# Performance work log

Measured on AMD Instinct MI355X. Metric: run time of the kernel, lower is better.

The kernel has to match this reference:

```python
import jax, jax.numpy as jnp
import numpy as np

B, A, NC, DIR, LMAX, MAXZ, NORB = 8, 64, 128, 4, 2, 10, 14
NF = NC * DIR * (2 * LMAX + 1)   # 2560
O2 = NORB * NORB                 # 196
AO = A * NORB                    # 896
LOG2 = float(np.log(2.0))

def ssp(v):  # spk shifted softplus
    return jax.nn.softplus(v) - LOG2

def setup_inputs():
    key = jax.random.key(0)
    ks = jax.random.split(key, 12)
    Z = jax.random.randint(ks[0], (B, A), 1, MAXZ)
    idx = np.arange(A)
    nbh_np = np.stack([np.delete(idx, i) for i in range(A)], 0)  # [A, A-1]: all atoms except self
    nbh = jnp.asarray(np.broadcast_to(nbh_np[None], (B, A, A - 1)).copy(), dtype=jnp.int32)
    x = jax.random.normal(ks[1], (B, A, NC), jnp.float32)
    Vijkl = jax.random.normal(ks[2], (B, A, A - 1, NF), jnp.float32) * 0.1
    sc = 1.0 / np.sqrt(NF)
    W_off = jax.random.normal(ks[3], (NF, O2), jnp.float32) * sc
    b_off = jnp.zeros((O2,), jnp.float32)
    W_on = jax.random.normal(ks[4], (NF, O2), jnp.float32) * sc
    b_on = jnp.zeros((O2,), jnp.float32)
    W_ovoff = jax.random.normal(ks[5], (NF, O2), jnp.float32) * sc
    b_ovoff = jnp.zeros((O2,), jnp.float32)
    ov_emb = jax.random.normal(ks[6], (MAXZ, O2), jnp.float32) * 0.1  # trainable overlap onsite embedding
    orb_energies = jax.random.normal(ks[7], (MAXZ, NORB), jnp.float32)  # h0 energies
    s0_energies = jnp.ones((MAXZ, NORB), jnp.float32)                   # s0 init = ones
    W1 = jax.random.normal(ks[8], (NC, NC // 2), jnp.float32) / np.sqrt(NC)
    b1 = jnp.zeros((NC // 2,), jnp.float32)
    W2 = jax.random.normal(ks[9], (NC // 2, 1), jnp.float32) / np.sqrt(NC // 2)
    b2 = jnp.zeros((1,), jnp.float32)
    return {"Z": Z, "nbh": nbh, "x": x, "Vijkl": Vijkl,
            "W_off": W_off, "b_off": b_off, "W_on": W_on, "b_on": b_on,
            "W_ovoff": W_ovoff, "b_ovoff": b_ovoff, "ov_emb": ov_emb,
            "orb_energies": orb_energies, "s0_energies": s0_energies,
            "W1": W1, "b1": b1, "W2": W2, "b2": b2}

def reference(Z, nbh, x, Vijkl, W_off, b_off, W_on, b_on, W_ovoff, b_ovoff,
              ov_emb, orb_energies, s0_energies, W1, b1, W2, b2):
    # permutation that reorders neighbor slots (plus appended zero/self slot) into atom order
    ar = jnp.broadcast_to(jnp.arange(A, dtype=nbh.dtype)[None, :, None], (B, A, 1))
    sort_idx = jnp.argsort(jnp.concatenate([nbh, ar], axis=2), axis=2)  # [B,A,A]
    eyeA = jnp.eye(A, dtype=Vijkl.dtype)
    eyeAO = jnp.eye(AO, dtype=Vijkl.dtype)

    def assemble(off, on):
        # off: [B,A,A-1,O2] pair blocks; on: [B,A,O2] onsite blocks
        offz = jnp.concatenate([off, jnp.zeros((B, A, 1, O2), off.dtype)], axis=2)  # zero self block at slot A-1
        offg = jnp.take_along_axis(offz, sort_idx[..., None], axis=2)               # [B,A,A,O2]
        M = offg + eyeA[None, :, :, None] * on[:, :, None, :]
        M = M.reshape(B, A, A, NORB, NORB).transpose(0, 1, 3, 2, 4).reshape(B, AO, AO)
        return 0.5 * (M + M.transpose(0, 2, 1))

    # Hamiltonian: offsite Dense + onsite Dense mean-aggregated over pairs
    H_off = Vijkl @ W_off + b_off                       # [B,A,A-1,O2]
    H_on = jnp.mean(Vijkl @ W_on + b_on, axis=2)        # [B,A,O2]
    H = assemble(H_off, H_on)
    # h0 single-atom diagonal (orb mask is all-active -> full diagonal)
    H = H + eyeAO[None] * orb_energies[Z].reshape(B, 1, AO)

    # Overlap: offsite Dense + onsite embedding lookup
    S_off = Vijkl @ W_ovoff + b_ovoff
    S_on = ov_emb[Z]                                    # [B,A,O2]
    S = assemble(S_off, S_on)
    S = S + eyeAO[None] * s0_energies[Z].reshape(B, 1, AO)

    # energy head: Dense->ssp->Dense->ScaleShift(0,1), sum over atoms
    Ei = ssp(x @ W1 + b1) @ W2 + b2                     # [B,A,1]
    E = jnp.sum(Ei, axis=1)                             # [B,1]
    return H, S, E
```

## Files before the change

kernel.cpp:

```cpp
#include <hip/hip_runtime.h>

#define B_      8
#define A_      64
#define NPAIR   63
#define NC_     128
#define NF_     2560
#define O2_     196
#define NORB_   14
#define AO_     896
#define NCOLS   588
#define NSTORE  392
#define CSTRIDE 400
#define KSTEPS  80
#define BM      126
#define BN      640
#define BSTEP_BYTES 40960

typedef short bf16x8 __attribute__((ext_vector_type(8)));
typedef float f32x4  __attribute__((ext_vector_type(4)));

__device__ __forceinline__ unsigned f2bf(float f) {
    unsigned u = __builtin_bit_cast(unsigned, f);
    return (u + 0x7fffu + ((u >> 16) & 1u)) >> 16;
}

__global__ __launch_bounds__(512)
void prep_energy(const float* __restrict__ W_off, const float* __restrict__ W_ovoff,
                 const float* __restrict__ W_on, unsigned short* __restrict__ Bws,
                 const float* __restrict__ x, const float* __restrict__ W1,
                 const float* __restrict__ b1, const float* __restrict__ W2,
                 const float* __restrict__ b2, float* __restrict__ E) {
    const int t = threadIdx.x;
    if (blockIdx.x < KSTEPS) {
        __shared__ float wt[32 * BN];
        const int ks = blockIdx.x;
        for (int e = t; e < 32 * BN; e += 512) {
            int kl = e / BN, c = e - kl * BN;
            int kg = ks * 32 + kl;
            float v = 0.f;
            if (c < O2_)          v = W_off  [(size_t)kg * O2_ + c];
            else if (c < 2 * O2_) v = W_ovoff[(size_t)kg * O2_ + (c - O2_)];
            else if (c < 3 * O2_) v = W_on   [(size_t)kg * O2_ + (c - 2 * O2_)];
            wt[kl * BN + c] = v;
        }
        __syncthreads();
        unsigned short* out = Bws + (size_t)ks * (BN * 32);
        for (int e = t; e < BN * 4; e += 512) {
            int n = e >> 2, sg = e & 3;
            uint4 w;
            w.x = f2bf(wt[(sg * 8 + 0) * BN + n]) | (f2bf(wt[(sg * 8 + 1) * BN + n]) << 16);
            w.y = f2bf(wt[(sg * 8 + 2) * BN + n]) | (f2bf(wt[(sg * 8 + 3) * BN + n]) << 16);
            w.z = f2bf(wt[(sg * 8 + 4) * BN + n]) | (f2bf(wt[(sg * 8 + 5) * BN + n]) << 16);
            w.w = f2bf(wt[(sg * 8 + 6) * BN + n]) | (f2bf(wt[(sg * 8 + 7) * BN + n]) << 16);
            *(uint4*)(out + (size_t)n * 32 + sg * 8) = w;
        }
    } else {
        __shared__ float partial[8];
        const int b = blockIdx.x - KSTEPS;
        const int lane = t & 63;
        const int w = t >> 6;
        float esum = 0.f;
        for (int aa = 0; aa < 8; ++aa) {
            const int a = w * 8 + aa;
            const float* xr = x + (size_t)(b * A_ + a) * NC_;
            float hj = b1[lane];
            for (int k = 0; k < NC_; ++k) hj = fmaf(xr[k], W1[k * 64 + lane], hj);
            float sp = fmaxf(hj, 0.f) + log1pf(expf(-fabsf(hj))) - 0.69314718055994531f;
            float v = sp * W2[lane];
            for (int off = 32; off; off >>= 1) v += __shfl_down(v, off);
            if (lane == 0) esum += v + b2[0];
        }
        if (lane == 0) partial[w] = esum;
        __syncthreads();
        if (t == 0) {
            float e = 0.f;
            for (int k = 0; k < 8; ++k) e += partial[k];
            E[b] = e;
        }
    }
}

__global__ __launch_bounds__(1024, 4)
void gemm_off(const float* __restrict__ V, const unsigned short* __restrict__ Bws,
              const float* __restrict__ b_off, const float* __restrict__ b_ovoff,
              const float* __restrict__ b_on, float* __restrict__ HSoff,
              float* __restrict__ Hon) {
    __shared__ alignas(16) float          Af32[4][4096];
    __shared__ alignas(16) unsigned short Ab16[3][4096];
    __shared__ float HonLds[2][O2_];

    const int tid  = threadIdx.x;
    const int mt   = blockIdx.x;
    const int lane = tid & 63;
    const int wv   = tid >> 6;
    const int wm   = wv >> 3, wn = wv & 7;
    const int wvu  = __builtin_amdgcn_readfirstlane(wv);
    const bool sthr = tid < BM * 8;

    const float* asrc = V + (size_t)(mt * BM + (tid >> 3)) * NF_ + (tid & 7) * 4;

    const char* bp = (const char*)Bws + (size_t)(wn * 80 + (lane & 15)) * 64 + (lane >> 4) * 16;
#define BFRAG(t_, nf_) (*(const bf16x8*)(bp + (size_t)(t_) * BSTEP_BYTES + (nf_) * 1024))

    f32x4 acc[4][5];
#pragma unroll
    for (int mf = 0; mf < 4; ++mf)
#pragma unroll
        for (int nf = 0; nf < 5; ++nf)
            acc[mf][nf] = (f32x4){0.f, 0.f, 0.f, 0.f};

    auto stage = [&](int slot, int kk) {
        if (sthr)
            __builtin_amdgcn_global_load_lds(
                (const __attribute__((address_space(1))) void*)(asrc + (size_t)kk * 32),
                (__attribute__((address_space(3))) void*)(&Af32[slot][wvu * 256]), 16, 0, 0);
    };

    const int crr = tid >> 3, cq = tid & 7;
    const int csl = ((cq >> 1) + ((crr + (crr >> 2)) & 3)) & 3;
    const unsigned cdst = (unsigned)(crr * 64 + csl * 16 + (cq & 1) * 8);
    auto conv = [&](int fslot, int bslot) {
        if (sthr) {
            float4 cf = *(const float4*)((const char*)&Af32[fslot][0] + tid * 16);
            unsigned lo, hi;
            asm("v_cvt_pk_bf16_f32 %0, %1, %2" : "=v"(lo) : "v"(cf.x), "v"(cf.y));
            asm("v_cvt_pk_bf16_f32 %0, %1, %2" : "=v"(hi) : "v"(cf.z), "v"(cf.w));
            uint2 cw = {lo, hi};
            *(uint2*)((char*)&Ab16[bslot][0] + cdst) = cw;
        }
    };

    const unsigned klo4 = (unsigned)(lane >> 4);
#define AFRAG(abf_, mf_, Bb16_) {                                                   \
    const unsigned R_ = (unsigned)(wm * 64 + (lane & 15) + (mf_) * 16);             \
    const unsigned sl_ = (klo4 + ((R_ + (R_ >> 2)) & 3)) & 3;                       \
    abf_ = *(const bf16x8*)((const char*)(Bb16_) + R_ * 64 + sl_ * 16); }

#define MFMA1(abf_, bq_, mf_, nf_) \
    acc[mf_][nf_] = __builtin_amdgcn_mfma_f32_16x16x32_bf16(abf_, bq_, acc[mf_][nf_], 0, 0, 0);

    bf16x8 bq0, bq1, bq2, bq3, bq4, abf;

    stage(0, 0); stage(1, 1); stage(2, 2); stage(3, 3);
    bq0 = BFRAG(0, 0); bq1 = BFRAG(0, 1); bq2 = BFRAG(0, 2); bq3 = BFRAG(0, 3); bq4 = BFRAG(0, 4);
    asm volatile("s_waitcnt vmcnt(8)" ::: "memory");
    __builtin_amdgcn_sched_barrier(0);
    conv(0, 0);
    asm volatile("s_waitcnt vmcnt(7)" ::: "memory");
    __builtin_amdgcn_sched_barrier(0);
    conv(1, 1);
    asm volatile("s_waitcnt lgkmcnt(0)" ::: "memory");
    __builtin_amdgcn_s_barrier();
    __builtin_amdgcn_sched_barrier(0);

    for (int t = 0; t < KSTEPS; ++t) {
        if (t + 2 < KSTEPS) {
            asm volatile("s_waitcnt vmcnt(6)" ::: "memory");
            __builtin_amdgcn_sched_barrier(0);
            conv((t + 2) & 3, (t + 2) % 3);
        }

        const unsigned short* At = &Ab16[t % 3][0];
#pragma unroll
        for (int mf = 0; mf < 4; ++mf) {
            AFRAG(abf, mf, At);
            __builtin_amdgcn_s_setprio(1);
            MFMA1(abf, bq0, mf, 0); if (mf == 3) bq0 = BFRAG(t + 1, 0);
            MFMA1(abf, bq1, mf, 1); if (mf == 3) bq1 = BFRAG(t + 1, 1);
            MFMA1(abf, bq2, mf, 2); if (mf == 3) bq2 = BFRAG(t + 1, 2);
            MFMA1(abf, bq3, mf, 3); if (mf == 3) bq3 = BFRAG(t + 1, 3);
            MFMA1(abf, bq4, mf, 4); if (mf == 3) bq4 = BFRAG(t + 1, 4);
            __builtin_amdgcn_s_setprio(0);
        }

        {
            int kk = t + 4 < KSTEPS ? t + 4 : KSTEPS - 1;
            stage((t + 4) & 3, kk);
        }
        asm volatile("s_waitcnt lgkmcnt(0)" ::: "memory");
        __builtin_amdgcn_sched_barrier(0);
        __builtin_amdgcn_s_barrier();
        __builtin_amdgcn_sched_barrier(0);
    }

    asm volatile("s_waitcnt vmcnt(0)" ::: "memory");
    if (tid < 2 * O2_) HonLds[tid / O2_][tid % O2_] = 0.f;
    __syncthreads();

    const int c16 = lane & 15, rg = lane >> 4;
#pragma unroll
    for (int nf = 0; nf < 5; ++nf) {
        const int C = wn * 80 + nf * 16 + c16;
        if (C >= NSTORE) continue;
        const float bias = (C < O2_) ? b_off[C] : b_ovoff[C - O2_];
#pragma unroll
        for (int mf = 0; mf < 4; ++mf) {
            const int L = wm * 64 + mf * 16 + rg * 4;
#pragma unroll
            for (int jj = 0; jj < 4; ++jj) {
                const int row = L + jj;
                if (row < BM)
                    HSoff[(size_t)(mt * BM + row) * CSTRIDE + C] = acc[mf][nf][jj] + bias;
            }
        }
    }
#pragma unroll
    for (int nf = 0; nf < 5; ++nf) {
        const int C = wn * 80 + nf * 16 + c16;
        if (C < NSTORE || C >= NCOLS) continue;
        const int cc = C - NSTORE;
        float s0 = 0.f, s1 = 0.f;
#pragma unroll
        for (int mf = 0; mf < 4; ++mf) {
            const int L = wm * 64 + mf * 16 + rg * 4;
#pragma unroll
            for (int jj = 0; jj < 4; ++jj) {
                const int row = L + jj;
                const float v = acc[mf][nf][jj];
                if (row < NPAIR)            s0 += v;
                else if (row < BM)          s1 += v;
            }
        }
        s0 += __shfl_down(s0, 32); s0 += __shfl_down(s0, 16);
        s1 += __shfl_down(s1, 32); s1 += __shfl_down(s1, 16);
        if (lane < 16) {
            atomicAdd(&HonLds[0][cc], s0);
            atomicAdd(&HonLds[1][cc], s1);
        }
    }
    __syncthreads();
    if (tid < 2 * O2_) {
        const int atom = tid / O2_, c = tid % O2_;
        Hon[(size_t)(mt * 2 + atom) * O2_ + c] =
            HonLds[atom][c] * (1.f / (float)NPAIR) + b_on[c];
    }
#undef BFRAG
#undef AFRAG
#undef MFMA1
}

__global__ __launch_bounds__(256)
void assemble_k(const float* __restrict__ HSoff, const float* __restrict__ Hon,
                const int* __restrict__ Z, const float* __restrict__ ov_emb,
                const float* __restrict__ orbE, const float* __restrict__ s0E,
                float* __restrict__ H, float* __restrict__ S) {
    __shared__ float Ai[NPAIR * 197];
    __shared__ float Bj[2][16 * 200];
    __shared__ float Dg[O2_];
    __shared__ float Dd[NORB_];

    const int bid = blockIdx.x;
    const int h = bid & 1, i = (bid >> 1) & 63, b = bid >> 7;
    const int t = threadIdx.x;
    const int g = b * A_ + i;
    const int z = Z[g];
    float* out = (h ? S : H) + (size_t)b * AO_ * AO_;

    const float* abase = HSoff + (size_t)g * NPAIR * CSTRIDE + h * O2_;
    for (int u = t; u < NPAIR * O2_; u += 256) {
        int jj = u / O2_, e = u - jj * O2_;
        Ai[jj * 197 + e] = abase[(size_t)jj * CSTRIDE + e];
    }
    if (t < O2_)   Dg[t] = h ? ov_emb[(size_t)z * O2_ + t]   : Hon[(size_t)g * O2_ + t];
    if (t < NORB_) Dd[t] = h ? s0E[(size_t)z * NORB_ + t]    : orbE[(size_t)z * NORB_ + t];

    auto stageB = [&](int buf, int jc) {
        for (int u = t; u < 16 * O2_; u += 256) {
            int jl = u / O2_, e = u - jl * O2_;
            int j = jc * 16 + jl;
            if (j != i) {
                int idx = (i < j) ? i : i - 1;
                Bj[buf][jl * 200 + e] =
                    HSoff[((size_t)(b * A_ + j) * NPAIR + idx) * CSTRIDE + h * O2_ + e];
            }
        }
    };
    stageB(0, 0);
    __syncthreads();

    const int tj = t / NORB_, tq = t - tj * NORB_;
    for (int jc = 0; jc < 4; ++jc) {
        if (jc < 3) stageB((jc + 1) & 1, jc + 1);
        if (t < 224) {
            const int j = jc * 16 + tj;
            const int cur = jc & 1;
#pragma unroll
            for (int p = 0; p < NORB_; ++p) {
                float v;
                if (j == i) {
                    v = 0.5f * (Dg[p * NORB_ + tq] + Dg[tq * NORB_ + p]);
                    if (p == tq) v += Dd[p];
                } else {
                    int jj = (j < i) ? j : j - 1;
                    v = 0.5f * (Ai[jj * 197 + p * NORB_ + tq] + Bj[cur][tj * 200 + tq * NORB_ + p]);
                }
                out[(size_t)(i * NORB_ + p) * AO_ + jc * 224 + t] = v;
            }
        }
        __syncthreads();
    }
}

extern "C" void kernel_launch(void* const* d_in, const int* in_sizes, int n_in,
                              void* d_out, int out_size, void* d_ws, size_t ws_size,
                              hipStream_t stream) {
    const int*   Z       = (const int*)  d_in[0];
    const float* x       = (const float*)d_in[2];
    const float* V       = (const float*)d_in[3];
    const float* W_off   = (const float*)d_in[4];
    const float* b_off   = (const float*)d_in[5];
    const float* W_on    = (const float*)d_in[6];
    const float* b_on    = (const float*)d_in[7];
    const float* W_ovoff = (const float*)d_in[8];
    const float* b_ovoff = (const float*)d_in[9];
    const float* ov_emb  = (const float*)d_in[10];
    const float* orbE    = (const float*)d_in[11];
    const float* s0E     = (const float*)d_in[12];
    const float* W1      = (const float*)d_in[13];
    const float* b1      = (const float*)d_in[14];
    const float* W2      = (const float*)d_in[15];
    const float* b2      = (const float*)d_in[16];

    float* H = (float*)d_out;
    float* S = H + (size_t)B_ * AO_ * AO_;
    float* E = S + (size_t)B_ * AO_ * AO_;

    char* ws = (char*)d_ws;
    unsigned short* Bws = (unsigned short*)ws;
    float* HSoff = (float*)(ws + (size_t)4  * 1024 * 1024);
    float* Hon   = (float*)(ws + (size_t)60 * 1024 * 1024);

    prep_energy<<<KSTEPS + B_, 512, 0, stream>>>(W_off, W_ovoff, W_on, Bws,
                                                 x, W1, b1, W2, b2, E);
    gemm_off   <<<256,  1024, 0, stream>>>(V, Bws, b_off, b_ovoff, b_on, HSoff, Hon);
    assemble_k <<<1024, 256,  0, stream>>>(HSoff, Hon, Z, ov_emb, orbE, s0E, H, S);
}
```

Measured before the change: 252.6 us.

## Load A fragments directly from global into registers, one atom per block

The GEMM kernel drops the LDS staging pipeline (global_load_lds, bf16 conversion into LDS, per-step barriers). Each wave now loads its fp32 A rows straight into registers, converts them to bf16 in registers, and feeds the MFMAs with one step of register prefetch. The M tile shrinks from 126 to 63 rows, so each block handles one atom, the grid doubles to 512 blocks, and blockIdx is remapped to spread blocks. This removes LDS traffic and barriers and raises parallelism, but each block still reloads all B fragments, rows padded past 63 are loaded redundantly, and global-load latency is hidden only by a single-step prefetch.

After: 573.8 us. 2.27x slower.

```diff
diff --git a/kernel.cpp b/kernel.cpp
--- a/kernel.cpp
+++ b/kernel.cpp
@@ -12,7 +12,6 @@
 #define NSTORE  392
 #define CSTRIDE 400
 #define KSTEPS  80
-#define BM      126
 #define BN      640
 #define BSTEP_BYTES 40960
 
@@ -85,106 +84,76 @@
               const float* __restrict__ b_off, const float* __restrict__ b_ovoff,
               const float* __restrict__ b_on, float* __restrict__ HSoff,
               float* __restrict__ Hon) {
-    __shared__ alignas(16) float          Af32[4][4096];
-    __shared__ alignas(16) unsigned short Ab16[3][4096];
-    __shared__ float HonLds[2][O2_];
+    __shared__ float HonLds[O2_];
 
     const int tid  = threadIdx.x;
-    const int mt   = blockIdx.x;
+    int mtb = blockIdx.x;
+    mtb = (mtb & 7) * 64 + (mtb >> 3);
+    const int mt   = mtb;
     const int lane = tid & 63;
     const int wv   = tid >> 6;
     const int wm   = wv >> 3, wn = wv & 7;
-    const int wvu  = __builtin_amdgcn_readfirstlane(wv);
-    const bool sthr = tid < BM * 8;
-
-    const float* asrc = V + (size_t)(mt * BM + (tid >> 3)) * NF_ + (tid & 7) * 4;
+
+    const int r0 = wm * 32 + (lane & 15);
+    const int rowA0 = mt * NPAIR + (r0      < NPAIR ? r0      : NPAIR - 1);
+    const int rowA1 = mt * NPAIR + (r0 + 16 < NPAIR ? r0 + 16 : NPAIR - 1);
+    const float* ap0 = V + (size_t)rowA0 * NF_ + (lane >> 4) * 8;
+    const float* ap1 = V + (size_t)rowA1 * NF_ + (lane >> 4) * 8;
 
     const char* bp = (const char*)Bws + (size_t)(wn * 80 + (lane & 15)) * 64 + (lane >> 4) * 16;
 #define BFRAG(t_, nf_) (*(const bf16x8*)(bp + (size_t)(t_) * BSTEP_BYTES + (nf_) * 1024))
 
-    f32x4 acc[4][5];
-#pragma unroll
-    for (int mf = 0; mf < 4; ++mf)
+    f32x4 acc[2][5];
+#pragma unroll
+    for (int mf = 0; mf < 2; ++mf)
 #pragma unroll
         for (int nf = 0; nf < 5; ++nf)
             acc[mf][nf] = (f32x4){0.f, 0.f, 0.f, 0.f};
 
-    auto stage = [&](int slot, int kk) {
-        if (sthr)
-            __builtin_amdgcn_global_load_lds(
-                (const __attribute__((address_space(1))) void*)(asrc + (size_t)kk * 32),
-                (__attribute__((address_space(3))) void*)(&Af32[slot][wvu * 256]), 16, 0, 0);
-    };
-
-    const int crr = tid >> 3, cq = tid & 7;
-    const int csl = ((cq >> 1) + ((crr + (crr >> 2)) & 3)) & 3;
-    const unsigned cdst = (unsigned)(crr * 64 + csl * 16 + (cq & 1) * 8);
-    auto conv = [&](int fslot, int bslot) {
-        if (sthr) {
-            float4 cf = *(const float4*)((const char*)&Af32[fslot][0] + tid * 16);
-            unsigned lo, hi;
-            asm("v_cvt_pk_bf16_f32 %0, %1, %2" : "=v"(lo) : "v"(cf.x), "v"(cf.y));
-            asm("v_cvt_pk_bf16_f32 %0, %1, %2" : "=v"(hi) : "v"(cf.z), "v"(cf.w));
-            uint2 cw = {lo, hi};
-            *(uint2*)((char*)&Ab16[bslot][0] + cdst) = cw;
-        }
-    };
-
-    const unsigned klo4 = (unsigned)(lane >> 4);
-#define AFRAG(abf_, mf_, Bb16_) {                                                   \
-    const unsigned R_ = (unsigned)(wm * 64 + (lane & 15) + (mf_) * 16);             \
-    const unsigned sl_ = (klo4 + ((R_ + (R_ >> 2)) & 3)) & 3;                       \
-    abf_ = *(const bf16x8*)((const char*)(Bb16_) + R_ * 64 + sl_ * 16); }
+    union U8 { unsigned u[4]; bf16x8 v; };
+#define CVT8(dst_, lo_, hi_) {                                                      \
+    U8 uu_;                                                                         \
+    asm("v_cvt_pk_bf16_f32 %0, %1, %2" : "=v"(uu_.u[0]) : "v"(lo_.x), "v"(lo_.y));  \
+    asm("v_cvt_pk_bf16_f32 %0, %1, %2" : "=v"(uu_.u[1]) : "v"(lo_.z), "v"(lo_.w));  \
+    asm("v_cvt_pk_bf16_f32 %0, %1, %2" : "=v"(uu_.u[2]) : "v"(hi_.x), "v"(hi_.y));  \
+    asm("v_cvt_pk_bf16_f32 %0, %1, %2" : "=v"(uu_.u[3]) : "v"(hi_.z), "v"(hi_.w));  \
+    dst_ = uu_.v; }
 
 #define MFMA1(abf_, bq_, mf_, nf_) \
     acc[mf_][nf_] = __builtin_amdgcn_mfma_f32_16x16x32_bf16(abf_, bq_, acc[mf_][nf_], 0, 0, 0);
 
-    bf16x8 bq0, bq1, bq2, bq3, bq4, abf;
-
-    stage(0, 0); stage(1, 1); stage(2, 2); stage(3, 3);
+    bf16x8 bq0, bq1, bq2, bq3, bq4, af0, af1;
+    float4 p0l, p0h, p1l, p1h;
+
+    p0l = ((const float4*)(ap0))[0]; p0h = ((const float4*)(ap0))[1];
+    p1l = ((const float4*)(ap1))[0]; p1h = ((const float4*)(ap1))[1];
     bq0 = BFRAG(0, 0); bq1 = BFRAG(0, 1); bq2 = BFRAG(0, 2); bq3 = BFRAG(0, 3); bq4 = BFRAG(0, 4);
-    asm volatile("s_waitcnt vmcnt(8)" ::: "memory");
-    __builtin_amdgcn_sched_barrier(0);
-    conv(0, 0);
-    asm volatile("s_waitcnt vmcnt(7)" ::: "memory");
-    __builtin_amdgcn_sched_barrier(0);
-    conv(1, 1);
-    asm volatile("s_waitcnt lgkmcnt(0)" ::: "memory");
-    __builtin_amdgcn_s_barrier();
-    __builtin_amdgcn_sched_barrier(0);
+    CVT8(af0, p0l, p0h);
+    CVT8(af1, p1l, p1h);
 
     for (int t = 0; t < KSTEPS; ++t) {
-        if (t + 2 < KSTEPS) {
-            asm volatile("s_waitcnt vmcnt(6)" ::: "memory");
-            __builtin_amdgcn_sched_barrier(0);
-            conv((t + 2) & 3, (t + 2) % 3);
-        }
-
-        const unsigned short* At = &Ab16[t % 3][0];
-#pragma unroll
-        for (int mf = 0; mf < 4; ++mf) {
-            AFRAG(abf, mf, At);
-            __builtin_amdgcn_s_setprio(1);
-            MFMA1(abf, bq0, mf, 0); if (mf == 3) bq0 = BFRAG(t + 1, 0);
-            MFMA1(abf, bq1, mf, 1); if (mf == 3) bq1 = BFRAG(t + 1, 1);
-            MFMA1(abf, bq2, mf, 2); if (mf == 3) bq2 = BFRAG(t + 1, 2);
-            MFMA1(abf, bq3, mf, 3); if (mf == 3) bq3 = BFRAG(t + 1, 3);
-            MFMA1(abf, bq4, mf, 4); if (mf == 3) bq4 = BFRAG(t + 1, 4);
-            __builtin_amdgcn_s_setprio(0);
-        }
-
-        {
-            int kk = t + 4 < KSTEPS ? t + 4 : KSTEPS - 1;
-            stage((t + 4) & 3, kk);
-        }
-        asm volatile("s_waitcnt lgkmcnt(0)" ::: "memory");
-        __builtin_amdgcn_sched_barrier(0);
-        __builtin_amdgcn_s_barrier();
-        __builtin_amdgcn_sched_barrier(0);
-    }
-
-    asm volatile("s_waitcnt vmcnt(0)" ::: "memory");
-    if (tid < 2 * O2_) HonLds[tid / O2_][tid % O2_] = 0.f;
+        const int tn = (t + 1 < KSTEPS) ? t + 1 : KSTEPS - 1;
+        const float* a0n = ap0 + (size_t)tn * 32;
+        const float* a1n = ap1 + (size_t)tn * 32;
+        p0l = ((const float4*)a0n)[0]; p0h = ((const float4*)a0n)[1];
+        p1l = ((const float4*)a1n)[0]; p1h = ((const float4*)a1n)[1];
+
+        MFMA1(af0, bq0, 0, 0);
+        MFMA1(af0, bq1, 0, 1);
+        MFMA1(af0, bq2, 0, 2);
+        MFMA1(af0, bq3, 0, 3);
+        MFMA1(af0, bq4, 0, 4);
+        MFMA1(af1, bq0, 1, 0); bq0 = BFRAG(tn, 0);
+        MFMA1(af1, bq1, 1, 1); bq1 = BFRAG(tn, 1);
+        MFMA1(af1, bq2, 1, 2); bq2 = BFRAG(tn, 2);
+        MFMA1(af1, bq3, 1, 3); bq3 = BFRAG(tn, 3);
+        MFMA1(af1, bq4, 1, 4); bq4 = BFRAG(tn, 4);
+
+        CVT8(af0, p0l, p0h);
+        CVT8(af1, p1l, p1h);
+    }
+
+    if (tid < O2_) HonLds[tid] = 0.f;
     __syncthreads();
 
     const int c16 = lane & 15, rg = lane >> 4;
@@ -194,13 +163,13 @@
         if (C >= NSTORE) continue;
         const float bias = (C < O2_) ? b_off[C] : b_ovoff[C - O2_];
 #pragma unroll
-        for (int mf = 0; mf < 4; ++mf) {
-            const int L = wm * 64 + mf * 16 + rg * 4;
+        for (int mf = 0; mf < 2; ++mf) {
+            const int L = wm * 32 + mf * 16 + rg * 4;
 #pragma unroll
             for (int jj = 0; jj < 4; ++jj) {
                 const int row = L + jj;
-                if (row < BM)
-                    HSoff[(size_t)(mt * BM + row) * CSTRIDE + C] = acc[mf][nf][jj] + bias;
+                if (row < NPAIR)
+                    HSoff[(size_t)(mt * NPAIR + row) * CSTRIDE + C] = acc[mf][nf][jj] + bias;
             }
         }
     }
@@ -209,33 +178,23 @@
         const int C = wn * 80 + nf * 16 + c16;
         if (C < NSTORE || C >= NCOLS) continue;
         const int cc = C - NSTORE;
-        float s0 = 0.f, s1 = 0.f;
-#pragma unroll
-        for (int mf = 0; mf < 4; ++mf) {
-            const int L = wm * 64 + mf * 16 + rg * 4;
-#pragma unroll
-            for (int jj = 0; jj < 4; ++jj) {
-                const int row = L + jj;
-                const float v = acc[mf][nf][jj];
-                if (row < NPAIR)            s0 += v;
-                else if (row < BM)          s1 += v;
-            }
-        }
-        s0 += __shfl_down(s0, 32); s0 += __shfl_down(s0, 16);
-        s1 += __shfl_down(s1, 32); s1 += __shfl_down(s1, 16);
-        if (lane < 16) {
-            atomicAdd(&HonLds[0][cc], s0);
-            atomicAdd(&HonLds[1][cc], s1);
-        }
+        float s = 0.f;
+#pragma unroll
+        for (int mf = 0; mf < 2; ++mf) {
+            const int L = wm * 32 + mf * 16 + rg * 4;
+#pragma unroll
+            for (int jj = 0; jj < 4; ++jj)
+                if (L + jj < NPAIR) s += acc[mf][nf][jj];
+        }
+        s += __shfl_down(s, 32);
+        s += __shfl_down(s, 16);
+        if (lane < 16) atomicAdd(&HonLds[cc], s);
     }
     __syncthreads();
-    if (tid < 2 * O2_) {
-        const int atom = tid / O2_, c = tid % O2_;
-        Hon[(size_t)(mt * 2 + atom) * O2_ + c] =
-            HonLds[atom][c] * (1.f / (float)NPAIR) + b_on[c];
-    }
+    if (tid < O2_)
+        Hon[(size_t)mt * O2_ + tid] = HonLds[tid] * (1.f / (float)NPAIR) + b_on[tid];
 #undef BFRAG
-#undef AFRAG
+#undef CVT8
 #undef MFMA1
 }
 
@@ -332,6 +291,6 @@
 
     prep_energy<<<KSTEPS + B_, 512, 0, stream>>>(W_off, W_ovoff, W_on, Bws,
                                                  x, W1, b1, W2, b2, E);
-    gemm_off   <<<256,  1024, 0, stream>>>(V, Bws, b_off, b_ovoff, b_on, HSoff, Hon);
+    gemm_off   <<<512,  1024, 0, stream>>>(V, Bws, b_off, b_ovoff, b_on, HSoff, Hon);
     assemble_k <<<1024, 256,  0, stream>>>(HSoff, Hon, Z, ov_emb, orbE, s0E, H, S);
 }
```

## Switch main GEMM from bf16 to scaled fp8 MFMA with 128-deep K macro-steps

Applied to the files above, without the earlier changes.

Converts both activations and weights to fp8 and runs the GEMM with scaled 16x16x128 fp8 MFMAs. The weights are pre-scaled by 8 and a scale exponent undoes that factor. The block shrinks to 512 threads with 10 N-fragments per wave, and A tiles are double-buffered in groups of four 32-wide K slices, giving 20 macro-iterations. The goal is higher MFMA throughput and fewer barriers per K. The cost is a large precision loss from fp8 that could break tolerance, plus more registers and LDS per block.

Result: slower. 288.2 us (+14.1%).

```diff
diff --git a/kernel.cpp b/kernel.cpp
--- a/kernel.cpp
+++ b/kernel.cpp
@@ -12,12 +12,17 @@
 #define NSTORE  392
 #define CSTRIDE 400
 #define KSTEPS  80
+#define NMACRO  20
 #define BM      126
 #define BN      640
-#define BSTEP_BYTES 40960
-
-typedef short bf16x8 __attribute__((ext_vector_type(8)));
-typedef float f32x4  __attribute__((ext_vector_type(4)));
+#define MAC_BYTES 81920
+
+typedef float f32x4 __attribute__((ext_vector_type(4)));
+typedef int   v8i   __attribute__((ext_vector_type(8)));
+typedef int   v4i   __attribute__((ext_vector_type(4)));
+
+#define SCA 0x7F7F7F7F
+#define SCB 0x7C7C7C7C
 
 __device__ __forceinline__ unsigned f2bf(float f) {
     unsigned u = __builtin_bit_cast(unsigned, f);
@@ -26,7 +31,7 @@
 
 __global__ __launch_bounds__(512)
 void prep_energy(const float* __restrict__ W_off, const float* __restrict__ W_ovoff,
-                 const float* __restrict__ W_on, unsigned short* __restrict__ Bws,
+                 const float* __restrict__ W_on, unsigned char* __restrict__ Bws,
                  const float* __restrict__ x, const float* __restrict__ W1,
                  const float* __restrict__ b1, const float* __restrict__ W2,
                  const float* __restrict__ b2, float* __restrict__ E) {
@@ -41,18 +46,15 @@
             if (c < O2_)          v = W_off  [(size_t)kg * O2_ + c];
             else if (c < 2 * O2_) v = W_ovoff[(size_t)kg * O2_ + (c - O2_)];
             else if (c < 3 * O2_) v = W_on   [(size_t)kg * O2_ + (c - 2 * O2_)];
-            wt[kl * BN + c] = v;
+            wt[kl * BN + c] = v * 8.0f;
         }
         __syncthreads();
-        unsigned short* out = Bws + (size_t)ks * (BN * 32);
-        for (int e = t; e < BN * 4; e += 512) {
-            int n = e >> 2, sg = e & 3;
-            uint4 w;
-            w.x = f2bf(wt[(sg * 8 + 0) * BN + n]) | (f2bf(wt[(sg * 8 + 1) * BN + n]) << 16);
-            w.y = f2bf(wt[(sg * 8 + 2) * BN + n]) | (f2bf(wt[(sg * 8 + 3) * BN + n]) << 16);
-            w.z = f2bf(wt[(sg * 8 + 4) * BN + n]) | (f2bf(wt[(sg * 8 + 5) * BN + n]) << 16);
-            w.w = f2bf(wt[(sg * 8 + 6) * BN + n]) | (f2bf(wt[(sg * 8 + 7) * BN + n]) << 16);
-            *(uint4*)(out + (size_t)n * 32 + sg * 8) = w;
+        unsigned char* out = Bws + (size_t)(ks >> 2) * MAC_BYTES + (ks & 3) * 32;
+        for (int u = t; u < BN * 8; u += 512) {
+            int n = u >> 3, q = u & 7;
+            int w = __builtin_amdgcn_cvt_pk_fp8_f32(wt[(q*4+0)*BN+n], wt[(q*4+1)*BN+n], 0, false);
+            w     = __builtin_amdgcn_cvt_pk_fp8_f32(wt[(q*4+2)*BN+n], wt[(q*4+3)*BN+n], w, true);
+            *(int*)(out + (size_t)n * 128 + q * 4) = w;
         }
     } else {
         __shared__ float partial[8];
@@ -80,117 +82,120 @@
     }
 }
 
-__global__ __launch_bounds__(1024, 4)
-void gemm_off(const float* __restrict__ V, const unsigned short* __restrict__ Bws,
+__global__ __launch_bounds__(512, 2)
+void gemm_off(const float* __restrict__ V, const unsigned char* __restrict__ Bws,
               const float* __restrict__ b_off, const float* __restrict__ b_ovoff,
               const float* __restrict__ b_on, float* __restrict__ HSoff,
               float* __restrict__ Hon) {
-    __shared__ alignas(16) float          Af32[4][4096];
-    __shared__ alignas(16) unsigned short Ab16[3][4096];
+    __shared__ alignas(16) float Af32[8][4096];
+    __shared__ alignas(16) unsigned char Afp8[4 * 6144];
     __shared__ float HonLds[2][O2_];
 
     const int tid  = threadIdx.x;
     const int mt   = blockIdx.x;
     const int lane = tid & 63;
     const int wv   = tid >> 6;
-    const int wm   = wv >> 3, wn = wv & 7;
+    const int wm   = wv >> 2, wn = wv & 3;
     const int wvu  = __builtin_amdgcn_readfirstlane(wv);
-    const bool sthr = tid < BM * 8;
-
-    const float* asrc = V + (size_t)(mt * BM + (tid >> 3)) * NF_ + (tid & 7) * 4;
-
-    const char* bp = (const char*)Bws + (size_t)(wn * 80 + (lane & 15)) * 64 + (lane >> 4) * 16;
-#define BFRAG(t_, nf_) (*(const bf16x8*)(bp + (size_t)(t_) * BSTEP_BYTES + (nf_) * 1024))
-
-    f32x4 acc[4][5];
+
+    const int r0  = tid >> 3;
+    const int r1c = (64 + r0) > 125 ? 125 : (64 + r0);
+    const int sg  = tid & 7;
+    const float* asrc0 = V + (size_t)(mt * BM + r0)  * NF_ + sg * 4;
+    const float* asrc1 = V + (size_t)(mt * BM + r1c) * NF_ + sg * 4;
+
+    const unsigned char* bbase = Bws + ((size_t)(wn * 160 + (lane & 15))) * 128 + (lane >> 4) * 32;
+#define BLD(T_, nf_) (*(const v8i*)(bbase + (size_t)(T_) * MAC_BYTES + (nf_) * 2048))
+
+    const unsigned aoff = (unsigned)(lane >> 4) * 6144 + (unsigned)(wm * 64 + (lane & 15)) * 48;
+
+    f32x4 acc[4][10];
 #pragma unroll
     for (int mf = 0; mf < 4; ++mf)
 #pragma unroll
-        for (int nf = 0; nf < 5; ++nf)
+        for (int nf = 0; nf < 10; ++nf)
             acc[mf][nf] = (f32x4){0.f, 0.f, 0.f, 0.f};
 
-    auto stage = [&](int slot, int kk) {
-        if (sthr)
-            __builtin_amdgcn_global_load_lds(
-                (const __attribute__((address_space(1))) void*)(asrc + (size_t)kk * 32),
-                (__attribute__((address_space(3))) void*)(&Af32[slot][wvu * 256]), 16, 0, 0);
+    auto stage = [&](int slot, int k32) {
+        __builtin_amdgcn_global_load_lds(
+            (const __attribute__((address_space(1))) void*)(asrc0 + (size_t)k32 * 32),
+            (__attribute__((address_space(3))) void*)(&Af32[slot][wvu * 256]), 16, 0, 0);
+        __builtin_amdgcn_global_load_lds(
+            (const __attribute__((address_space(1))) void*)(asrc1 + (size_t)k32 * 32),
+            (__attribute__((address_space(3))) void*)(&Af32[slot][2048 + wvu * 256]), 16, 0, 0);
     };
-
-    const int crr = tid >> 3, cq = tid & 7;
-    const int csl = ((cq >> 1) + ((crr + (crr >> 2)) & 3)) & 3;
-    const unsigned cdst = (unsigned)(crr * 64 + csl * 16 + (cq & 1) * 8);
-    auto conv = [&](int fslot, int bslot) {
-        if (sthr) {
-            float4 cf = *(const float4*)((const char*)&Af32[fslot][0] + tid * 16);
-            unsigned lo, hi;
-            asm("v_cvt_pk_bf16_f32 %0, %1, %2" : "=v"(lo) : "v"(cf.x), "v"(cf.y));
-            asm("v_cvt_pk_bf16_f32 %0, %1, %2" : "=v"(hi) : "v"(cf.z), "v"(cf.w));
-            uint2 cw = {lo, hi};
-            *(uint2*)((char*)&Ab16[bslot][0] + cdst) = cw;
-        }
+    auto conv = [&](int slot, int sub) {
+        const char* sp = (const char*)&Af32[slot][0];
+        float4 f0 = *(const float4*)(sp + tid * 16);
+        float4 f1 = *(const float4*)(sp + tid * 16 + 8192);
+        int w0 = __builtin_amdgcn_cvt_pk_fp8_f32(f0.x, f0.y, 0, false);
+        w0     = __builtin_amdgcn_cvt_pk_fp8_f32(f0.z, f0.w, w0, true);
+        int w1 = __builtin_amdgcn_cvt_pk_fp8_f32(f1.x, f1.y, 0, false);
+        w1     = __builtin_amdgcn_cvt_pk_fp8_f32(f1.z, f1.w, w1, true);
+        *(int*)&Afp8[sub * 6144 + (tid >> 3) * 48 + (tid & 7) * 4] = w0;
+        *(int*)&Afp8[sub * 6144 + (64 + (tid >> 3)) * 48 + (tid & 7) * 4] = w1;
     };
 
-    const unsigned klo4 = (unsigned)(lane >> 4);
-#define AFRAG(abf_, mf_, Bb16_) {                                                   \
-    const unsigned R_ = (unsigned)(wm * 64 + (lane & 15) + (mf_) * 16);             \
-    const unsigned sl_ = (klo4 + ((R_ + (R_ >> 2)) & 3)) & 3;                       \
-    abf_ = *(const bf16x8*)((const char*)(Bb16_) + R_ * 64 + sl_ * 16); }
+    union AV { v4i h[2]; v8i v; };
+#define AFLD(dst_, mf_) { AV a_; \
+    a_.h[0] = *(const v4i*)&Afp8[aoff + (mf_) * 768];      \
+    a_.h[1] = *(const v4i*)&Afp8[aoff + (mf_) * 768 + 16]; \
+    dst_ = a_.v; }
 
 #define MFMA1(abf_, bq_, mf_, nf_) \
-    acc[mf_][nf_] = __builtin_amdgcn_mfma_f32_16x16x32_bf16(abf_, bq_, acc[mf_][nf_], 0, 0, 0);
-
-    bf16x8 bq0, bq1, bq2, bq3, bq4, abf;
+    acc[mf_][nf_] = __builtin_amdgcn_mfma_scale_f32_16x16x128_f8f6f4( \
+        abf_, bq_, acc[mf_][nf_], 0, 0, 0, SCA, 0, SCB);
+
+#define C4(bv_, nf_) { \
+    __builtin_amdgcn_s_setprio(1); \
+    MFMA1(af0, bv_, 0, nf_); MFMA1(af1, bv_, 1, nf_); \
+    MFMA1(af2, bv_, 2, nf_); MFMA1(af3, bv_, 3, nf_); \
+    __builtin_amdgcn_s_setprio(0); }
+
+    v8i b0, b1, b2, b3, b4, af0, af1, af2, af3;
 
     stage(0, 0); stage(1, 1); stage(2, 2); stage(3, 3);
-    bq0 = BFRAG(0, 0); bq1 = BFRAG(0, 1); bq2 = BFRAG(0, 2); bq3 = BFRAG(0, 3); bq4 = BFRAG(0, 4);
-    asm volatile("s_waitcnt vmcnt(8)" ::: "memory");
-    __builtin_amdgcn_sched_barrier(0);
-    conv(0, 0);
-    asm volatile("s_waitcnt vmcnt(7)" ::: "memory");
-    __builtin_amdgcn_sched_barrier(0);
-    conv(1, 1);
-    asm volatile("s_waitcnt lgkmcnt(0)" ::: "memory");
-    __builtin_amdgcn_s_barrier();
-    __builtin_amdgcn_sched_barrier(0);
-
-    for (int t = 0; t < KSTEPS; ++t) {
-        if (t + 2 < KSTEPS) {
-            asm volatile("s_waitcnt vmcnt(6)" ::: "memory");
+    b0 = BLD(0, 0); b1 = BLD(0, 1); b2 = BLD(0, 2); b3 = BLD(0, 3); b4 = BLD(0, 4);
+
+    for (int T = 0; T < NMACRO; ++T) {
+        const int sb = (T & 1) * 4;
+        const int st = ((T + 1) & 1) * 4;
+#pragma unroll
+        for (int i = 0; i < 4; ++i) {
+            asm volatile("s_waitcnt vmcnt(16)" ::: "memory");
             __builtin_amdgcn_sched_barrier(0);
-            conv((t + 2) & 3, (t + 2) % 3);
-        }
-
-        const unsigned short* At = &Ab16[t % 3][0];
-#pragma unroll
-        for (int mf = 0; mf < 4; ++mf) {
-            AFRAG(abf, mf, At);
-            __builtin_amdgcn_s_setprio(1);
-            MFMA1(abf, bq0, mf, 0); if (mf == 3) bq0 = BFRAG(t + 1, 0);
-            MFMA1(abf, bq1, mf, 1); if (mf == 3) bq1 = BFRAG(t + 1, 1);
-            MFMA1(abf, bq2, mf, 2); if (mf == 3) bq2 = BFRAG(t + 1, 2);
-            MFMA1(abf, bq3, mf, 3); if (mf == 3) bq3 = BFRAG(t + 1, 3);
-            MFMA1(abf, bq4, mf, 4); if (mf == 3) bq4 = BFRAG(t + 1, 4);
-            __builtin_amdgcn_s_setprio(0);
-        }
-
-        {
-            int kk = t + 4 < KSTEPS ? t + 4 : KSTEPS - 1;
-            stage((t + 4) & 3, kk);
+            if (T < NMACRO - 1) stage(st + i, 4 * (T + 1) + i);
+            else                stage(st + i, 76 + i);
+            conv(sb + i, i);
         }
         asm volatile("s_waitcnt lgkmcnt(0)" ::: "memory");
         __builtin_amdgcn_sched_barrier(0);
         __builtin_amdgcn_s_barrier();
         __builtin_amdgcn_sched_barrier(0);
-    }
-
-    asm volatile("s_waitcnt vmcnt(0)" ::: "memory");
+
+        AFLD(af0, 0); AFLD(af1, 1); AFLD(af2, 2); AFLD(af3, 3);
+        C4(b0, 0); b0 = BLD(T, 5);
+        C4(b1, 1); b1 = BLD(T, 6);
+        C4(b2, 2); b2 = BLD(T, 7);
+        C4(b3, 3); b3 = BLD(T, 8);
+        C4(b4, 4); b4 = BLD(T, 9);
+        C4(b0, 5); b0 = BLD(T + 1, 0);
+        C4(b1, 6); b1 = BLD(T + 1, 1);
+        C4(b2, 7); b2 = BLD(T + 1, 2);
+        C4(b3, 8); b3 = BLD(T + 1, 3);
+        C4(b4, 9); b4 = BLD(T + 1, 4);
+        __builtin_amdgcn_sched_barrier(0);
+        __builtin_amdgcn_s_barrier();
+        __builtin_amdgcn_sched_barrier(0);
+    }
+
     if (tid < 2 * O2_) HonLds[tid / O2_][tid % O2_] = 0.f;
     __syncthreads();
 
     const int c16 = lane & 15, rg = lane >> 4;
 #pragma unroll
-    for (int nf = 0; nf < 5; ++nf) {
-        const int C = wn * 80 + nf * 16 + c16;
+    for (int nf = 0; nf < 10; ++nf) {
+        const int C = wn * 160 + nf * 16 + c16;
         if (C >= NSTORE) continue;
         const float bias = (C < O2_) ? b_off[C] : b_ovoff[C - O2_];
 #pragma unroll
@@ -205,8 +210,8 @@
         }
     }
 #pragma unroll
-    for (int nf = 0; nf < 5; ++nf) {
-        const int C = wn * 80 + nf * 16 + c16;
+    for (int nf = 0; nf < 10; ++nf) {
+        const int C = wn * 160 + nf * 16 + c16;
         if (C < NSTORE || C >= NCOLS) continue;
         const int cc = C - NSTORE;
         float s0 = 0.f, s1 = 0.f;
@@ -217,8 +222,8 @@
             for (int jj = 0; jj < 4; ++jj) {
                 const int row = L + jj;
                 const float v = acc[mf][nf][jj];
-                if (row < NPAIR)            s0 += v;
-                else if (row < BM)          s1 += v;
+                if (row < NPAIR)       s0 += v;
+                else if (row < BM)     s1 += v;
             }
         }
         s0 += __shfl_down(s0, 32); s0 += __shfl_down(s0, 16);
@@ -234,9 +239,10 @@
         Hon[(size_t)(mt * 2 + atom) * O2_ + c] =
             HonLds[atom][c] * (1.f / (float)NPAIR) + b_on[c];
     }
-#undef BFRAG
-#undef AFRAG
+#undef BLD
+#undef AFLD
 #undef MFMA1
+#undef C4
 }
 
 __global__ __launch_bounds__(256)
@@ -326,12 +332,12 @@
     float* E = S + (size_t)B_ * AO_ * AO_;
 
     char* ws = (char*)d_ws;
-    unsigned short* Bws = (unsigned short*)ws;
+    unsigned char* Bws = (unsigned char*)ws;
     float* HSoff = (float*)(ws + (size_t)4  * 1024 * 1024);
     float* Hon   = (float*)(ws + (size_t)60 * 1024 * 1024);
 
     prep_energy<<<KSTEPS + B_, 512, 0, stream>>>(W_off, W_ovoff, W_on, Bws,
                                                  x, W1, b1, W2, b2, E);
-    gemm_off   <<<256,  1024, 0, stream>>>(V, Bws, b_off, b_ovoff, b_on, HSoff, Hon);
-    assemble_k <<<1024, 256,  0, stream>>>(HSoff, Hon, Z, ov_emb, orbE, s0E, H, S);
-}
+    gemm_off   <<<256,  512, 0, stream>>>(V, Bws, b_off, b_ovoff, b_on, HSoff, Hon);
+    assemble_k <<<1024, 256, 0, stream>>>(HSoff, Hon, Z, ov_emb, orbE, s0E, H, S);
+}
```
